# Kernel tuning notes

Hardware: AMD Instinct MI355X
Metric: run time of the kernel (lower is better)

Reference implementation:

```python
import jax, jax.numpy as jnp
import numpy as np

N_NODES = 50000
N_EDGES = 800000
FEAT = 256
HID = 64
OUT = 40


def setup_inputs() -> dict:
    key = jax.random.key(0)
    ks = jax.random.split(key, 5)
    x = jax.random.normal(ks[0], (N_NODES, FEAT), dtype=jnp.float32)
    edge_index = jax.random.randint(ks[1], (2, N_EDGES), 0, N_NODES, dtype=jnp.int64)
    # Glorot-style init for GCN linear weights
    W1 = jax.random.normal(ks[2], (FEAT, HID), dtype=jnp.float32) * (1.0 / np.sqrt(FEAT))
    b1 = jnp.zeros((HID,), dtype=jnp.float32)
    W2 = jax.random.normal(ks[3], (HID, OUT), dtype=jnp.float32) * (1.0 / np.sqrt(HID))
    b2 = jnp.zeros((OUT,), dtype=jnp.float32)
    return {"x": x, "edge_index": edge_index, "W1": W1, "b1": b1, "W2": W2, "b2": b2}


def _gcn_conv(h, W, b, src, dst, norm, n_nodes):
    # GCNConv: linear transform first (reduces message width), then
    # symmetric-normalized gather-scale-scatter aggregation.
    h = h @ W  # [N, out]
    msg = h[src] * norm[:, None]  # [E+N, out] gather + scale
    agg = jax.ops.segment_sum(msg, dst, num_segments=n_nodes)  # scatter-add
    return agg + b


def reference(x, edge_index, W1, b1, W2, b2):
    n = x.shape[0]
    # add self loops (GCNConv default add_self_loops=True)
    loops = jnp.arange(n, dtype=edge_index.dtype)
    src = jnp.concatenate([edge_index[0], loops])
    dst = jnp.concatenate([edge_index[1], loops])
    # symmetric normalization: deg computed on A + I (in-degree at dst)
    deg = jax.ops.segment_sum(jnp.ones_like(dst, dtype=x.dtype), dst, num_segments=n)
    dinv = jax.lax.rsqrt(deg)  # deg >= 1 due to self loops
    norm = dinv[src] * dinv[dst]  # [E+N]

    h = jax.nn.relu(_gcn_conv(x, W1, b1, src, dst, norm, n))
    # dropout is identity in eval mode (reference baseline)
    h = _gcn_conv(h, W2, b2, src, dst, norm, n)
    return jax.nn.log_softmax(h, axis=1)
```

## Files before the change

kernel.cpp:

```cpp
#include <hip/hip_runtime.h>
#include <hip/hip_bf16.h>


constexpr int NN   = 50000;
constexpr int NE   = 800000;
constexpr int FEAT = 256;
constexpr int HID  = 64;
constexpr int OUTD = 40;
constexpr int NC   = (NN + 255) / 256;
constexpr int FCH  = 2048;
constexpr int NCH  = (NE + FCH - 1) / FCH;

typedef short bf16x8 __attribute__((ext_vector_type(8)));
typedef float f32x4  __attribute__((ext_vector_type(4)));

__device__ __forceinline__ float b2f(__hip_bfloat16 v) { return __bfloat162float(v); }
__device__ __forceinline__ float bflo(unsigned u) { return __uint_as_float(u << 16); }
__device__ __forceinline__ float bfhi(unsigned u) { return __uint_as_float(u & 0xffff0000u); }
__device__ __forceinline__ unsigned short f2bu(float f) {
    __hip_bfloat16 h = __float2bfloat16(f);
    return *(unsigned short*)&h;
}
__device__ __forceinline__ unsigned pack2bf(float a, float b) {
    return (unsigned)f2bu(a) | ((unsigned)f2bu(b) << 16);
}
__device__ __forceinline__ float loadF(const void* p, int i, bool f32) {
    return f32 ? ((const float*)p)[i] : b2f(((const __hip_bfloat16*)p)[i]);
}
__device__ __forceinline__ int loadE(const int* ei, int e, int row, bool i64) {
    long long idx = (long long)row * NE + e;
    return i64 ? ei[2 * idx] : ei[idx];
}
__device__ __forceinline__ bf16x8 pack8(float4 a, float4 b) {
    bf16x8 r;
    r[0] = (short)f2bu(a.x); r[1] = (short)f2bu(a.y);
    r[2] = (short)f2bu(a.z); r[3] = (short)f2bu(a.w);
    r[4] = (short)f2bu(b.x); r[5] = (short)f2bu(b.y);
    r[6] = (short)f2bu(b.z); r[7] = (short)f2bu(b.w);
    return r;
}

__global__ __launch_bounds__(256) void k_zero(const unsigned* __restrict__ xw,
                                              const int* __restrict__ ew,
                                              int* flags, int* cnt) {
    int i = blockIdx.x * 256 + threadIdx.x;
    if (i < NN) cnt[i] = 0;
    if (blockIdx.x == 0 && threadIdx.x == 0) {
        int outliers = 0;
        for (int k = 0; k < 256; k++) {
            int e = (xw[k] >> 7) & 0xFF;
            if (e < 100 || e > 140) outliers++;
        }
        flags[0] = (outliers > 64) ? 1 : 0;
        int nz = 0;
        for (int k = 1; k < 64; k += 2)
            if (ew[k] != 0) nz++;
        flags[1] = (nz == 0) ? 1 : 0;
    }
}

__global__ __launch_bounds__(256) void k_hist(const int* __restrict__ ei,
                                              const int* __restrict__ flags,
                                              int* cnt, int* __restrict__ rank) {
    const bool i64 = flags[1] != 0;
    int e = blockIdx.x * 256 + threadIdx.x;
    if (e < NE) rank[e] = atomicAdd(&cnt[loadE(ei, e, 1, i64)], 1);
}
__global__ __launch_bounds__(256) void k_scan1(const int* __restrict__ cnt,
                                               int* row_start, int* partial, float* dinv) {
    __shared__ int s[256];
    int t = threadIdx.x, i = blockIdx.x * 256 + t;
    int v = (i < NN) ? cnt[i] : 0;
    if (i < NN) dinv[i] = rsqrtf(1.0f + (float)v);
    s[t] = v;
    __syncthreads();
    for (int off = 1; off < 256; off <<= 1) {
        int tmp = (t >= off) ? s[t - off] : 0;
        __syncthreads();
        s[t] += tmp;
        __syncthreads();
    }
    if (i < NN) row_start[i] = s[t] - v;
    if (t == 255) partial[blockIdx.x] = s[255];
}
__global__ __launch_bounds__(256) void k_scan3(int* row_start, const int* __restrict__ partial) {
    __shared__ int red[4];
    const int t = threadIdx.x;
    int v = (t < NC && t < (int)blockIdx.x) ? partial[t] : 0;
#pragma unroll
    for (int off = 32; off; off >>= 1) v += __shfl_xor(v, off, 64);
    if ((t & 63) == 0) red[t >> 6] = v;
    __syncthreads();
    int total = red[0] + red[1] + red[2] + red[3];
    int i = blockIdx.x * 256 + t;
    if (i < NN) row_start[i] += total;
}
__global__ __launch_bounds__(256) void k_fill(const int* __restrict__ ei,
                                              const int* __restrict__ flags,
                                              const int* __restrict__ row_start,
                                              const int* __restrict__ rank,
                                              unsigned short* __restrict__ csr16) {
    const bool i64 = flags[1] != 0;
    const int cls = blockIdx.x & 7;
    const int e0 = (blockIdx.x >> 3) * FCH;
#pragma unroll
    for (int k = 0; k < FCH / 256; k++) {
        int e = e0 + k * 256 + threadIdx.x;
        if (e < NE) {
            int d = loadE(ei, e, 1, i64);
            if (d / 6250 == cls) {
                int s = loadE(ei, e, 0, i64);
                csr16[row_start[d] + rank[e]] = (unsigned short)s;
            }
        }
    }
}

__global__ __launch_bounds__(256) void k_gemm1(const void* __restrict__ xb,
                                               const void* __restrict__ W1,
                                               const float* __restrict__ dinv,
                                               const int* __restrict__ flags,
                                               unsigned short* __restrict__ h1u) {
    __shared__ __align__(16) unsigned short wt16[64 * 264];
    const bool f32 = flags[0] != 0;
    const int t = threadIdx.x;
    if (f32) {
        const float* wf = (const float*)W1;
        for (int i = t * 4; i < FEAT * HID; i += 1024) {
            float4 w = *(const float4*)(wf + i);
            int k = i >> 6, n0 = i & 63;
            wt16[(n0 + 0) * 264 + k] = f2bu(w.x);
            wt16[(n0 + 1) * 264 + k] = f2bu(w.y);
            wt16[(n0 + 2) * 264 + k] = f2bu(w.z);
            wt16[(n0 + 3) * 264 + k] = f2bu(w.w);
        }
    } else {
        const unsigned short* wu = (const unsigned short*)W1;
        for (int i = t * 4; i < FEAT * HID; i += 1024) {
            ushort4 w = *(const ushort4*)(wu + i);
            int k = i >> 6, n0 = i & 63;
            wt16[(n0 + 0) * 264 + k] = w.x;
            wt16[(n0 + 1) * 264 + k] = w.y;
            wt16[(n0 + 2) * 264 + k] = w.z;
            wt16[(n0 + 3) * 264 + k] = w.w;
        }
    }
    const int wv = t >> 6, lane = t & 63, l15 = lane & 15, quad = lane >> 4;
    const int gr = blockIdx.x * 64 + wv * 16 + l15;
    const bool rowok = gr < NN;
    f32x4 acc[4];
#pragma unroll
    for (int nt = 0; nt < 4; nt++) acc[nt] = (f32x4){0.f, 0.f, 0.f, 0.f};
    __syncthreads();

    if (f32) {
        const float* xr = (const float*)xb + (size_t)gr * FEAT + quad * 8;
        float4 z4 = make_float4(0, 0, 0, 0);
        float4 c0 = rowok ? *(const float4*)xr : z4;
        float4 c1 = rowok ? *(const float4*)(xr + 4) : z4;
#pragma unroll
        for (int ks = 0; ks < 8; ks++) {
            float4 n0 = z4, n1 = z4;
            if (ks < 7 && rowok) {
                n0 = *(const float4*)(xr + (ks + 1) * 32);
                n1 = *(const float4*)(xr + (ks + 1) * 32 + 4);
            }
            bf16x8 a = pack8(c0, c1);
            const unsigned short* wk = wt16 + ks * 32 + quad * 8;
#pragma unroll
            for (int nt = 0; nt < 4; nt++) {
                bf16x8 b = *(const bf16x8*)(wk + (size_t)(nt * 16 + l15) * 264);
                acc[nt] = __builtin_amdgcn_mfma_f32_16x16x32_bf16(a, b, acc[nt], 0, 0, 0);
            }
            c0 = n0; c1 = n1;
        }
    } else {
        const unsigned short* xr = (const unsigned short*)xb + (size_t)gr * FEAT + quad * 8;
        bf16x8 zz = (bf16x8){0, 0, 0, 0, 0, 0, 0, 0};
        bf16x8 cur = rowok ? *(const bf16x8*)xr : zz;
#pragma unroll
        for (int ks = 0; ks < 8; ks++) {
            bf16x8 nxt = zz;
            if (ks < 7 && rowok) nxt = *(const bf16x8*)(xr + (ks + 1) * 32);
            const unsigned short* wk = wt16 + ks * 32 + quad * 8;
#pragma unroll
            for (int nt = 0; nt < 4; nt++) {
                bf16x8 b = *(const bf16x8*)(wk + (size_t)(nt * 16 + l15) * 264);
                acc[nt] = __builtin_amdgcn_mfma_f32_16x16x32_bf16(cur, b, acc[nt], 0, 0, 0);
            }
            cur = nxt;
        }
    }
    const int rbase = blockIdx.x * 64 + wv * 16 + quad * 4;
    float dv[4];
#pragma unroll
    for (int r = 0; r < 4; r++) dv[r] = (rbase + r < NN) ? dinv[rbase + r] : 0.f;
#pragma unroll
    for (int r = 0; r < 4; r++) {
        int grow = rbase + r;
        if (grow < NN) {
#pragma unroll
            for (int nt = 0; nt < 4; nt++)
                h1u[(size_t)grow * HID + nt * 16 + l15] = f2bu(acc[nt][r] * dv[r]);
        }
    }
}

__global__ __launch_bounds__(256) void k_gather1f(const uint2* __restrict__ h1v,
                                                  const float* __restrict__ dinv,
                                                  const int* __restrict__ row_start,
                                                  const int* __restrict__ cnt,
                                                  const unsigned short* __restrict__ csr16,
                                                  const void* __restrict__ W2,
                                                  const void* __restrict__ b1,
                                                  const int* __restrict__ flags,
                                                  unsigned short* __restrict__ h2u) {
    __shared__ __align__(16) float w2t[OUTD * 68];
    __shared__ __align__(16) float gbuf[16 * 68];
    __shared__ float dns[16];
    const bool f32 = flags[0] != 0;
    const int t = threadIdx.x;
    for (int i = t; i < HID * OUTD; i += 256) {
        int c = i >> 6, k = i & 63;
        w2t[c * 68 + k] = loadF(W2, (size_t)k * OUTD + c, f32);
    }
    const int nl = t >> 4, l16 = t & 15;
    const int n = blockIdx.x * 16 + nl;
    const float dn = dinv[n];
    uint2 u0 = h1v[(size_t)n * 16 + l16];
    float a00 = bflo(u0.x), a01 = bfhi(u0.x), a02 = bflo(u0.y), a03 = bfhi(u0.y);
    float a10 = 0.f, a11 = 0.f, a12 = 0.f, a13 = 0.f;
    float a20 = 0.f, a21 = 0.f, a22 = 0.f, a23 = 0.f;
    float a30 = 0.f, a31 = 0.f, a32 = 0.f, a33 = 0.f;
    const int rs = row_start[n], c = cnt[n];
    for (int base = 0; base < c; base += 16) {
        int m = min(16, c - base);
        int sv = (l16 < m) ? (int)csr16[rs + base + l16] : 0;
        int j = 0;
        for (; j + 8 <= m; j += 8) {
            int s0 = __shfl(sv, j, 16),     s1 = __shfl(sv, j + 1, 16);
            int s2 = __shfl(sv, j + 2, 16), s3 = __shfl(sv, j + 3, 16);
            int s4 = __shfl(sv, j + 4, 16), s5 = __shfl(sv, j + 5, 16);
            int s6 = __shfl(sv, j + 6, 16), s7 = __shfl(sv, j + 7, 16);
            uint2 b0 = h1v[(size_t)s0 * 16 + l16];
            uint2 b1v_ = h1v[(size_t)s1 * 16 + l16];
            uint2 b2v = h1v[(size_t)s2 * 16 + l16];
            uint2 b3 = h1v[(size_t)s3 * 16 + l16];
            uint2 b4 = h1v[(size_t)s4 * 16 + l16];
            uint2 b5 = h1v[(size_t)s5 * 16 + l16];
            uint2 b6 = h1v[(size_t)s6 * 16 + l16];
            uint2 b7 = h1v[(size_t)s7 * 16 + l16];
            a00 += bflo(b0.x); a01 += bfhi(b0.x); a02 += bflo(b0.y); a03 += bfhi(b0.y);
            a10 += bflo(b1v_.x); a11 += bfhi(b1v_.x); a12 += bflo(b1v_.y); a13 += bfhi(b1v_.y);
            a20 += bflo(b2v.x); a21 += bfhi(b2v.x); a22 += bflo(b2v.y); a23 += bfhi(b2v.y);
            a30 += bflo(b3.x); a31 += bfhi(b3.x); a32 += bflo(b3.y); a33 += bfhi(b3.y);
            a00 += bflo(b4.x); a01 += bfhi(b4.x); a02 += bflo(b4.y); a03 += bfhi(b4.y);
            a10 += bflo(b5.x); a11 += bfhi(b5.x); a12 += bflo(b5.y); a13 += bfhi(b5.y);
            a20 += bflo(b6.x); a21 += bfhi(b6.x); a22 += bflo(b6.y); a23 += bfhi(b6.y);
            a30 += bflo(b7.x); a31 += bfhi(b7.x); a32 += bflo(b7.y); a33 += bfhi(b7.y);
        }
        for (; j < m; j++) {
            int s0 = __shfl(sv, j, 16);
            uint2 b0 = h1v[(size_t)s0 * 16 + l16];
            a00 += bflo(b0.x); a01 += bfhi(b0.x); a02 += bflo(b0.y); a03 += bfhi(b0.y);
        }
    }
    int cb = 4 * l16;
    float g0 = fmaxf(dn * (a00 + a10 + a20 + a30) + loadF(b1, cb, f32), 0.f);
    float g1 = fmaxf(dn * (a01 + a11 + a21 + a31) + loadF(b1, cb + 1, f32), 0.f);
    float g2 = fmaxf(dn * (a02 + a12 + a22 + a32) + loadF(b1, cb + 2, f32), 0.f);
    float g3 = fmaxf(dn * (a03 + a13 + a23 + a33) + loadF(b1, cb + 3, f32), 0.f);
    *(float4*)(gbuf + nl * 68 + cb) = make_float4(g0, g1, g2, g3);
    if (l16 == 0) dns[nl] = dn;
    __syncthreads();
    for (int idx = t; idx < 16 * OUTD; idx += 256) {
        int node = idx / OUTD, col = idx % OUTD;
        const float4* gp = (const float4*)(gbuf + node * 68);
        const float4* wp = (const float4*)(w2t + col * 68);
        float o = 0.f;
#pragma unroll 4
        for (int k4 = 0; k4 < 16; k4++) {
            float4 a = gp[k4], b = wp[k4];
            o += a.x * b.x + a.y * b.y + a.z * b.z + a.w * b.w;
        }
        h2u[(size_t)(blockIdx.x * 16 + node) * OUTD + col] = f2bu(o * dns[node]);
    }
}

__global__ __launch_bounds__(256) void k_gather2(const uint2* __restrict__ h2v,
                                                 const float* __restrict__ dinv,
                                                 const int* __restrict__ row_start,
                                                 const int* __restrict__ cnt,
                                                 const unsigned short* __restrict__ csr16,
                                                 const void* __restrict__ b2,
                                                 const int* __restrict__ flags,
                                                 void* __restrict__ out) {
    const bool f32 = flags[0] != 0;
    const int t = threadIdx.x;
    const int nl = t >> 4, l16 = t & 15;
    const int n = blockIdx.x * 16 + nl;
    const bool act = l16 < 10;
    const float dn = dinv[n];
    uint2 u0 = act ? h2v[(size_t)n * 10 + l16] : make_uint2(0, 0);
    float a00 = bflo(u0.x), a01 = bfhi(u0.x), a02 = bflo(u0.y), a03 = bfhi(u0.y);
    float a10 = 0.f, a11 = 0.f, a12 = 0.f, a13 = 0.f;
    float a20 = 0.f, a21 = 0.f, a22 = 0.f, a23 = 0.f;
    float a30 = 0.f, a31 = 0.f, a32 = 0.f, a33 = 0.f;
    const int rs = row_start[n], c = cnt[n];
    for (int base = 0; base < c; base += 16) {
        int m = min(16, c - base);
        int sv = (l16 < m) ? (int)csr16[rs + base + l16] : 0;
        int j = 0;
        for (; j + 8 <= m; j += 8) {
            int s0 = __shfl(sv, j, 16),     s1 = __shfl(sv, j + 1, 16);
            int s2 = __shfl(sv, j + 2, 16), s3 = __shfl(sv, j + 3, 16);
            int s4 = __shfl(sv, j + 4, 16), s5 = __shfl(sv, j + 5, 16);
            int s6 = __shfl(sv, j + 6, 16), s7 = __shfl(sv, j + 7, 16);
            if (act) {
                uint2 b0 = h2v[(size_t)s0 * 10 + l16];
                uint2 b1v_ = h2v[(size_t)s1 * 10 + l16];
                uint2 b2v = h2v[(size_t)s2 * 10 + l16];
                uint2 b3 = h2v[(size_t)s3 * 10 + l16];
                uint2 b4 = h2v[(size_t)s4 * 10 + l16];
                uint2 b5 = h2v[(size_t)s5 * 10 + l16];
                uint2 b6 = h2v[(size_t)s6 * 10 + l16];
                uint2 b7 = h2v[(size_t)s7 * 10 + l16];
                a00 += bflo(b0.x); a01 += bfhi(b0.x); a02 += bflo(b0.y); a03 += bfhi(b0.y);
                a10 += bflo(b1v_.x); a11 += bfhi(b1v_.x); a12 += bflo(b1v_.y); a13 += bfhi(b1v_.y);
                a20 += bflo(b2v.x); a21 += bfhi(b2v.x); a22 += bflo(b2v.y); a23 += bfhi(b2v.y);
                a30 += bflo(b3.x); a31 += bfhi(b3.x); a32 += bflo(b3.y); a33 += bfhi(b3.y);
                a00 += bflo(b4.x); a01 += bfhi(b4.x); a02 += bflo(b4.y); a03 += bfhi(b4.y);
                a10 += bflo(b5.x); a11 += bfhi(b5.x); a12 += bflo(b5.y); a13 += bfhi(b5.y);
                a20 += bflo(b6.x); a21 += bfhi(b6.x); a22 += bflo(b6.y); a23 += bfhi(b6.y);
                a30 += bflo(b7.x); a31 += bfhi(b7.x); a32 += bflo(b7.y); a33 += bfhi(b7.y);
            }
        }
        for (; j < m; j++) {
            int s0 = __shfl(sv, j, 16);
            if (act) {
                uint2 b0 = h2v[(size_t)s0 * 10 + l16];
                a00 += bflo(b0.x); a01 += bfhi(b0.x); a02 += bflo(b0.y); a03 += bfhi(b0.y);
            }
        }
    }
    int cb = 4 * l16;
    float v0 = -3.0e38f, v1 = -3.0e38f, v2 = -3.0e38f, v3 = -3.0e38f;
    if (act) {
        v0 = dn * (a00 + a10 + a20 + a30) + loadF(b2, cb, f32);
        v1 = dn * (a01 + a11 + a21 + a31) + loadF(b2, cb + 1, f32);
        v2 = dn * (a02 + a12 + a22 + a32) + loadF(b2, cb + 2, f32);
        v3 = dn * (a03 + a13 + a23 + a33) + loadF(b2, cb + 3, f32);
    }
    float mx = fmaxf(fmaxf(v0, v1), fmaxf(v2, v3));
#pragma unroll
    for (int off = 8; off; off >>= 1) mx = fmaxf(mx, __shfl_xor(mx, off, 16));
    float ev = act ? expf(v0 - mx) + expf(v1 - mx) + expf(v2 - mx) + expf(v3 - mx) : 0.f;
#pragma unroll
    for (int off = 8; off; off >>= 1) ev += __shfl_xor(ev, off, 16);
    float lg = logf(ev);
    if (act) {
        float r0 = v0 - mx - lg, r1 = v1 - mx - lg;
        float r2 = v2 - mx - lg, r3 = v3 - mx - lg;
        if (f32) {
            *(float4*)((float*)out + (size_t)n * OUTD + cb) = make_float4(r0, r1, r2, r3);
        } else {
            ((uint2*)out)[(size_t)n * 10 + l16] = make_uint2(pack2bf(r0, r1), pack2bf(r2, r3));
        }
    }
}

extern "C" void kernel_launch(void* const* d_in, const int* in_sizes, int n_in,
                              void* d_out, int out_size, void* d_ws, size_t ws_size,
                              hipStream_t stream) {
    const void* x  = d_in[0];
    const int*  ei = (const int*)d_in[1];
    const void* W1 = d_in[2];
    const void* b1 = d_in[3];
    const void* W2 = d_in[4];
    const void* b2 = d_in[5];

    float* ws        = (float*)d_ws;
    int*   flags     = (int*)ws;
    float* dinv      = ws + 16;
    int*   cnt       = (int*)(dinv + 50048);
    int*   row_start = cnt + 50048;
    int*   partial   = row_start + 50048;
    int*   rank      = partial + 256;
    unsigned short* csr16 = (unsigned short*)(rank + NE);
    unsigned short* h1u   = csr16 + NE;
    unsigned short* h2u   = h1u + (size_t)NN * HID;

    k_zero  <<<(NN + 255) / 256, 256, 0, stream>>>((const unsigned*)x, ei, flags, cnt);
    k_hist  <<<(NE + 255) / 256, 256, 0, stream>>>(ei, flags, cnt, rank);
    k_scan1 <<<NC, 256, 0, stream>>>(cnt, row_start, partial, dinv);
    k_scan3 <<<NC, 256, 0, stream>>>(row_start, partial);
    k_fill  <<<NCH * 8, 256, 0, stream>>>(ei, flags, row_start, rank, csr16);
    k_gemm1 <<<(NN + 63) / 64, 256, 0, stream>>>(x, W1, dinv, flags, h1u);
    k_gather1f<<<NN / 16, 256, 0, stream>>>((const uint2*)h1u, dinv, row_start, cnt, csr16,
                                            W2, b1, flags, h2u);
    k_gather2<<<NN / 16, 256, 0, stream>>>((const uint2*)h2u, dinv, row_start, cnt, csr16,
                                           b2, flags, d_out);
}
```

Measured before the change: 237.5 us.

## Use zero-row padding for branchless 16-wide gathers and single-block partial scan

The gather loops now always issue 16 neighbour loads per chunk. Unused slots point at a padded zero row (index 50000) in h1/h2, which replaces the 8-wide plus scalar tail loops with fixed unrolled loads and two accumulator sets. The multi-block scan3 kernel is replaced by a one-block scan of the partials, and consumers add pp[d>>8] instead of rewriting row_start. This costs extra wasted loads for low-degree nodes and relies on gemm1 writing padded rows whose dinv is zero, in exchange for more memory-level parallelism and less divergence.

```diff
diff --git a/kernel.cpp b/kernel.cpp
--- a/kernel.cpp
+++ b/kernel.cpp
@@ -3,6 +3,8 @@
 
 
 constexpr int NN   = 50000;
+constexpr int NNP  = 50048;
+constexpr int ZR   = 50000;
 constexpr int NE   = 800000;
 constexpr int FEAT = 256;
 constexpr int HID  = 64;
@@ -42,9 +44,11 @@
 
 __global__ __launch_bounds__(256) void k_zero(const unsigned* __restrict__ xw,
                                               const int* __restrict__ ew,
-                                              int* flags, int* cnt) {
+                                              int* flags, int* cnt,
+                                              unsigned* __restrict__ h2pad) {
     int i = blockIdx.x * 256 + threadIdx.x;
     if (i < NN) cnt[i] = 0;
+    if (blockIdx.x == 0 && threadIdx.x < 20) h2pad[threadIdx.x] = 0;
     if (blockIdx.x == 0 && threadIdx.x == 0) {
         int outliers = 0;
         for (int k = 0; k < 256; k++) {
@@ -83,21 +87,24 @@
     if (i < NN) row_start[i] = s[t] - v;
     if (t == 255) partial[blockIdx.x] = s[255];
 }
-__global__ __launch_bounds__(256) void k_scan3(int* row_start, const int* __restrict__ partial) {
-    __shared__ int red[4];
-    const int t = threadIdx.x;
-    int v = (t < NC && t < (int)blockIdx.x) ? partial[t] : 0;
-#pragma unroll
-    for (int off = 32; off; off >>= 1) v += __shfl_xor(v, off, 64);
-    if ((t & 63) == 0) red[t >> 6] = v;
+__global__ __launch_bounds__(256) void k_scan2p(const int* __restrict__ partial, int* pp) {
+    __shared__ int s[256];
+    int t = threadIdx.x;
+    int v = (t < NC) ? partial[t] : 0;
+    s[t] = v;
     __syncthreads();
-    int total = red[0] + red[1] + red[2] + red[3];
-    int i = blockIdx.x * 256 + t;
-    if (i < NN) row_start[i] += total;
+    for (int off = 1; off < 256; off <<= 1) {
+        int tmp = (t >= off) ? s[t - off] : 0;
+        __syncthreads();
+        s[t] += tmp;
+        __syncthreads();
+    }
+    pp[t] = s[t] - v;
 }
 __global__ __launch_bounds__(256) void k_fill(const int* __restrict__ ei,
                                               const int* __restrict__ flags,
                                               const int* __restrict__ row_start,
+                                              const int* __restrict__ pp,
                                               const int* __restrict__ rank,
                                               unsigned short* __restrict__ csr16) {
     const bool i64 = flags[1] != 0;
@@ -110,7 +117,7 @@
             int d = loadE(ei, e, 1, i64);
             if (d / 6250 == cls) {
                 int s = loadE(ei, e, 0, i64);
-                csr16[row_start[d] + rank[e]] = (unsigned short)s;
+                csr16[row_start[d] + pp[d >> 8] + rank[e]] = (unsigned short)s;
             }
         }
     }
@@ -198,17 +205,16 @@
 #pragma unroll
     for (int r = 0; r < 4; r++) {
         int grow = rbase + r;
-        if (grow < NN) {
-#pragma unroll
-            for (int nt = 0; nt < 4; nt++)
-                h1u[(size_t)grow * HID + nt * 16 + l15] = f2bu(acc[nt][r] * dv[r]);
-        }
+#pragma unroll
+        for (int nt = 0; nt < 4; nt++)
+            h1u[(size_t)grow * HID + nt * 16 + l15] = f2bu(acc[nt][r] * dv[r]);
     }
 }
 
 __global__ __launch_bounds__(256) void k_gather1f(const uint2* __restrict__ h1v,
                                                   const float* __restrict__ dinv,
                                                   const int* __restrict__ row_start,
+                                                  const int* __restrict__ pp,
                                                   const int* __restrict__ cnt,
                                                   const unsigned short* __restrict__ csr16,
                                                   const void* __restrict__ W2,
@@ -228,48 +234,36 @@
     const int n = blockIdx.x * 16 + nl;
     const float dn = dinv[n];
     uint2 u0 = h1v[(size_t)n * 16 + l16];
-    float a00 = bflo(u0.x), a01 = bfhi(u0.x), a02 = bflo(u0.y), a03 = bfhi(u0.y);
-    float a10 = 0.f, a11 = 0.f, a12 = 0.f, a13 = 0.f;
-    float a20 = 0.f, a21 = 0.f, a22 = 0.f, a23 = 0.f;
-    float a30 = 0.f, a31 = 0.f, a32 = 0.f, a33 = 0.f;
-    const int rs = row_start[n], c = cnt[n];
+    float a0 = bflo(u0.x), a1 = bfhi(u0.x), a2 = bflo(u0.y), a3 = bfhi(u0.y);
+    float e0 = 0.f, e1 = 0.f, e2 = 0.f, e3 = 0.f;
+    const int rs = row_start[n] + pp[n >> 8], c = cnt[n];
     for (int base = 0; base < c; base += 16) {
-        int m = min(16, c - base);
-        int sv = (l16 < m) ? (int)csr16[rs + base + l16] : 0;
-        int j = 0;
-        for (; j + 8 <= m; j += 8) {
-            int s0 = __shfl(sv, j, 16),     s1 = __shfl(sv, j + 1, 16);
-            int s2 = __shfl(sv, j + 2, 16), s3 = __shfl(sv, j + 3, 16);
-            int s4 = __shfl(sv, j + 4, 16), s5 = __shfl(sv, j + 5, 16);
-            int s6 = __shfl(sv, j + 6, 16), s7 = __shfl(sv, j + 7, 16);
-            uint2 b0 = h1v[(size_t)s0 * 16 + l16];
-            uint2 b1v_ = h1v[(size_t)s1 * 16 + l16];
-            uint2 b2v = h1v[(size_t)s2 * 16 + l16];
-            uint2 b3 = h1v[(size_t)s3 * 16 + l16];
-            uint2 b4 = h1v[(size_t)s4 * 16 + l16];
-            uint2 b5 = h1v[(size_t)s5 * 16 + l16];
-            uint2 b6 = h1v[(size_t)s6 * 16 + l16];
-            uint2 b7 = h1v[(size_t)s7 * 16 + l16];
-            a00 += bflo(b0.x); a01 += bfhi(b0.x); a02 += bflo(b0.y); a03 += bfhi(b0.y);
-            a10 += bflo(b1v_.x); a11 += bfhi(b1v_.x); a12 += bflo(b1v_.y); a13 += bfhi(b1v_.y);
-            a20 += bflo(b2v.x); a21 += bfhi(b2v.x); a22 += bflo(b2v.y); a23 += bfhi(b2v.y);
-            a30 += bflo(b3.x); a31 += bfhi(b3.x); a32 += bflo(b3.y); a33 += bfhi(b3.y);
-            a00 += bflo(b4.x); a01 += bfhi(b4.x); a02 += bflo(b4.y); a03 += bfhi(b4.y);
-            a10 += bflo(b5.x); a11 += bfhi(b5.x); a12 += bflo(b5.y); a13 += bfhi(b5.y);
-            a20 += bflo(b6.x); a21 += bfhi(b6.x); a22 += bflo(b6.y); a23 += bfhi(b6.y);
-            a30 += bflo(b7.x); a31 += bfhi(b7.x); a32 += bflo(b7.y); a33 += bfhi(b7.y);
-        }
-        for (; j < m; j++) {
-            int s0 = __shfl(sv, j, 16);
-            uint2 b0 = h1v[(size_t)s0 * 16 + l16];
-            a00 += bflo(b0.x); a01 += bfhi(b0.x); a02 += bflo(b0.y); a03 += bfhi(b0.y);
+        int rem = c - base;
+        int sv = (l16 < rem) ? (int)csr16[rs + base + l16] : ZR;
+        uint2 b[8], d[8];
+#pragma unroll
+        for (int j = 0; j < 8; j++) {
+            int s = __shfl(sv, j, 16);
+            b[j] = h1v[(size_t)s * 16 + l16];
+        }
+#pragma unroll
+        for (int j = 0; j < 8; j++) {
+            int s = __shfl(sv, j + 8, 16);
+            d[j] = h1v[(size_t)s * 16 + l16];
+        }
+#pragma unroll
+        for (int j = 0; j < 8; j++) {
+            a0 += bflo(b[j].x); a1 += bfhi(b[j].x);
+            a2 += bflo(b[j].y); a3 += bfhi(b[j].y);
+            e0 += bflo(d[j].x); e1 += bfhi(d[j].x);
+            e2 += bflo(d[j].y); e3 += bfhi(d[j].y);
         }
     }
     int cb = 4 * l16;
-    float g0 = fmaxf(dn * (a00 + a10 + a20 + a30) + loadF(b1, cb, f32), 0.f);
-    float g1 = fmaxf(dn * (a01 + a11 + a21 + a31) + loadF(b1, cb + 1, f32), 0.f);
-    float g2 = fmaxf(dn * (a02 + a12 + a22 + a32) + loadF(b1, cb + 2, f32), 0.f);
-    float g3 = fmaxf(dn * (a03 + a13 + a23 + a33) + loadF(b1, cb + 3, f32), 0.f);
+    float g0 = fmaxf(dn * (a0 + e0) + loadF(b1, cb, f32), 0.f);
+    float g1 = fmaxf(dn * (a1 + e1) + loadF(b1, cb + 1, f32), 0.f);
+    float g2 = fmaxf(dn * (a2 + e2) + loadF(b1, cb + 2, f32), 0.f);
+    float g3 = fmaxf(dn * (a3 + e3) + loadF(b1, cb + 3, f32), 0.f);
     *(float4*)(gbuf + nl * 68 + cb) = make_float4(g0, g1, g2, g3);
     if (l16 == 0) dns[nl] = dn;
     __syncthreads();
@@ -290,6 +284,7 @@
 __global__ __launch_bounds__(256) void k_gather2(const uint2* __restrict__ h2v,
                                                  const float* __restrict__ dinv,
                                                  const int* __restrict__ row_start,
+                                                 const int* __restrict__ pp,
                                                  const int* __restrict__ cnt,
                                                  const unsigned short* __restrict__ csr16,
                                                  const void* __restrict__ b2,
@@ -301,55 +296,40 @@
     const int n = blockIdx.x * 16 + nl;
     const bool act = l16 < 10;
     const float dn = dinv[n];
-    uint2 u0 = act ? h2v[(size_t)n * 10 + l16] : make_uint2(0, 0);
-    float a00 = bflo(u0.x), a01 = bfhi(u0.x), a02 = bflo(u0.y), a03 = bfhi(u0.y);
-    float a10 = 0.f, a11 = 0.f, a12 = 0.f, a13 = 0.f;
-    float a20 = 0.f, a21 = 0.f, a22 = 0.f, a23 = 0.f;
-    float a30 = 0.f, a31 = 0.f, a32 = 0.f, a33 = 0.f;
-    const int rs = row_start[n], c = cnt[n];
+    const int lclamp = act ? l16 : 9;
+    uint2 u0 = h2v[(size_t)n * 10 + lclamp];
+    float a0 = bflo(u0.x), a1 = bfhi(u0.x), a2 = bflo(u0.y), a3 = bfhi(u0.y);
+    float e0 = 0.f, e1 = 0.f, e2 = 0.f, e3 = 0.f;
+    const int rs = row_start[n] + pp[n >> 8], c = cnt[n];
     for (int base = 0; base < c; base += 16) {
-        int m = min(16, c - base);
-        int sv = (l16 < m) ? (int)csr16[rs + base + l16] : 0;
-        int j = 0;
-        for (; j + 8 <= m; j += 8) {
-            int s0 = __shfl(sv, j, 16),     s1 = __shfl(sv, j + 1, 16);
-            int s2 = __shfl(sv, j + 2, 16), s3 = __shfl(sv, j + 3, 16);
-            int s4 = __shfl(sv, j + 4, 16), s5 = __shfl(sv, j + 5, 16);
-            int s6 = __shfl(sv, j + 6, 16), s7 = __shfl(sv, j + 7, 16);
-            if (act) {
-                uint2 b0 = h2v[(size_t)s0 * 10 + l16];
-                uint2 b1v_ = h2v[(size_t)s1 * 10 + l16];
-                uint2 b2v = h2v[(size_t)s2 * 10 + l16];
-                uint2 b3 = h2v[(size_t)s3 * 10 + l16];
-                uint2 b4 = h2v[(size_t)s4 * 10 + l16];
-                uint2 b5 = h2v[(size_t)s5 * 10 + l16];
-                uint2 b6 = h2v[(size_t)s6 * 10 + l16];
-                uint2 b7 = h2v[(size_t)s7 * 10 + l16];
-                a00 += bflo(b0.x); a01 += bfhi(b0.x); a02 += bflo(b0.y); a03 += bfhi(b0.y);
-                a10 += bflo(b1v_.x); a11 += bfhi(b1v_.x); a12 += bflo(b1v_.y); a13 += bfhi(b1v_.y);
-                a20 += bflo(b2v.x); a21 += bfhi(b2v.x); a22 += bflo(b2v.y); a23 += bfhi(b2v.y);
-                a30 += bflo(b3.x); a31 += bfhi(b3.x); a32 += bflo(b3.y); a33 += bfhi(b3.y);
-                a00 += bflo(b4.x); a01 += bfhi(b4.x); a02 += bflo(b4.y); a03 += bfhi(b4.y);
-                a10 += bflo(b5.x); a11 += bfhi(b5.x); a12 += bflo(b5.y); a13 += bfhi(b5.y);
-                a20 += bflo(b6.x); a21 += bfhi(b6.x); a22 += bflo(b6.y); a23 += bfhi(b6.y);
-                a30 += bflo(b7.x); a31 += bfhi(b7.x); a32 += bflo(b7.y); a33 += bfhi(b7.y);
-            }
-        }
-        for (; j < m; j++) {
-            int s0 = __shfl(sv, j, 16);
-            if (act) {
-                uint2 b0 = h2v[(size_t)s0 * 10 + l16];
-                a00 += bflo(b0.x); a01 += bfhi(b0.x); a02 += bflo(b0.y); a03 += bfhi(b0.y);
-            }
+        int rem = c - base;
+        int sv = (l16 < rem) ? (int)csr16[rs + base + l16] : ZR;
+        uint2 b[8], d[8];
+#pragma unroll
+        for (int j = 0; j < 8; j++) {
+            int s = __shfl(sv, j, 16);
+            b[j] = h2v[(size_t)s * 10 + lclamp];
+        }
+#pragma unroll
+        for (int j = 0; j < 8; j++) {
+            int s = __shfl(sv, j + 8, 16);
+            d[j] = h2v[(size_t)s * 10 + lclamp];
+        }
+#pragma unroll
+        for (int j = 0; j < 8; j++) {
+            a0 += bflo(b[j].x); a1 += bfhi(b[j].x);
+            a2 += bflo(b[j].y); a3 += bfhi(b[j].y);
+            e0 += bflo(d[j].x); e1 += bfhi(d[j].x);
+            e2 += bflo(d[j].y); e3 += bfhi(d[j].y);
         }
     }
     int cb = 4 * l16;
     float v0 = -3.0e38f, v1 = -3.0e38f, v2 = -3.0e38f, v3 = -3.0e38f;
     if (act) {
-        v0 = dn * (a00 + a10 + a20 + a30) + loadF(b2, cb, f32);
-        v1 = dn * (a01 + a11 + a21 + a31) + loadF(b2, cb + 1, f32);
-        v2 = dn * (a02 + a12 + a22 + a32) + loadF(b2, cb + 2, f32);
-        v3 = dn * (a03 + a13 + a23 + a33) + loadF(b2, cb + 3, f32);
+        v0 = dn * (a0 + e0) + loadF(b2, cb, f32);
+        v1 = dn * (a1 + e1) + loadF(b2, cb + 1, f32);
+        v2 = dn * (a2 + e2) + loadF(b2, cb + 2, f32);
+        v3 = dn * (a3 + e3) + loadF(b2, cb + 3, f32);
     }
     float mx = fmaxf(fmaxf(v0, v1), fmaxf(v2, v3));
 #pragma unroll
@@ -385,19 +365,21 @@
     int*   cnt       = (int*)(dinv + 50048);
     int*   row_start = cnt + 50048;
     int*   partial   = row_start + 50048;
-    int*   rank      = partial + 256;
+    int*   pp        = partial + 256;
+    int*   rank      = pp + 256;
     unsigned short* csr16 = (unsigned short*)(rank + NE);
     unsigned short* h1u   = csr16 + NE;
-    unsigned short* h2u   = h1u + (size_t)NN * HID;
-
-    k_zero  <<<(NN + 255) / 256, 256, 0, stream>>>((const unsigned*)x, ei, flags, cnt);
+    unsigned short* h2u   = h1u + (size_t)NNP * HID;
+    unsigned* h2pad = (unsigned*)(h2u + (size_t)ZR * OUTD);
+
+    k_zero  <<<(NN + 255) / 256, 256, 0, stream>>>((const unsigned*)x, ei, flags, cnt, h2pad);
     k_hist  <<<(NE + 255) / 256, 256, 0, stream>>>(ei, flags, cnt, rank);
     k_scan1 <<<NC, 256, 0, stream>>>(cnt, row_start, partial, dinv);
-    k_scan3 <<<NC, 256, 0, stream>>>(row_start, partial);
-    k_fill  <<<NCH * 8, 256, 0, stream>>>(ei, flags, row_start, rank, csr16);
-    k_gemm1 <<<(NN + 63) / 64, 256, 0, stream>>>(x, W1, dinv, flags, h1u);
-    k_gather1f<<<NN / 16, 256, 0, stream>>>((const uint2*)h1u, dinv, row_start, cnt, csr16,
+    k_scan2p<<<1, 256, 0, stream>>>(partial, pp);
+    k_fill  <<<NCH * 8, 256, 0, stream>>>(ei, flags, row_start, pp, rank, csr16);
+    k_gemm1 <<<NNP / 64, 256, 0, stream>>>(x, W1, dinv, flags, h1u);
+    k_gather1f<<<NN / 16, 256, 0, stream>>>((const uint2*)h1u, dinv, row_start, pp, cnt, csr16,
                                             W2, b1, flags, h2u);
-    k_gather2<<<NN / 16, 256, 0, stream>>>((const uint2*)h2u, dinv, row_start, cnt, csr16,
+    k_gather2<<<NN / 16, 256, 0, stream>>>((const uint2*)h2u, dinv, row_start, pp, cnt, csr16,
                                            b2, flags, d_out);
 }
```

After: 230.1 us. 1.03x faster.
